# Performance work log

Measured on AMD Instinct MI355X. Metric: run time of the kernel, lower is better.

The kernel has to match this reference:

```python
import jax, jax.numpy as jnp
import numpy as np

M, N, D = 100000, 64, 128  # points, channels, voxel grid side


def setup_inputs() -> dict:
    key = jax.random.key(0)
    k1, k2, k3, k4, k5 = jax.random.split(key, 5)
    rng = np.random.default_rng(0)
    # unique occupied voxels in a D^3 grid (Minkowski coords are unique)
    lin = rng.choice(D ** 3, size=M, replace=False)
    coords = np.stack(np.unravel_index(lin, (D, D, D)), axis=1).astype(np.int32)
    w_scale = 0.02  # ~1/sqrt(fan_in=27*N)
    return {
        "feats": jax.random.normal(k1, (M, N), dtype=jnp.float32),
        "W1": jax.random.normal(k2, (27, N, N), dtype=jnp.float32) * w_scale,
        "b1": jax.random.normal(k3, (N,), dtype=jnp.float32) * 0.01,
        "W2": jax.random.normal(k4, (27, N, N), dtype=jnp.float32) * w_scale,
        "b2": jax.random.normal(k5, (N,), dtype=jnp.float32) * 0.01,
        "coords": jnp.asarray(coords),
        "grid_size": D,
    }


def reference(feats, W1, b1, W2, b2, coords, grid_size):
    Dg = grid_size
    m = feats.shape[0]
    # dense hash: linear voxel id -> point index (-1 if empty)
    lin = (coords[:, 0].astype(jnp.int32) * Dg + coords[:, 1]) * Dg + coords[:, 2]
    lookup = jnp.full((Dg * Dg * Dg,), -1, dtype=jnp.int32).at[lin].set(
        jnp.arange(m, dtype=jnp.int32))
    offsets = jnp.array([[i, j, k] for i in (-1, 0, 1) for j in (-1, 0, 1)
                         for k in (-1, 0, 1)], dtype=jnp.int32)  # [27,3]

    def sparse_conv(x, W, b):
        # out[u] = b + sum_k W_k^T gather(x, u+off_k); scan over 27 offsets keeps
        # only one [M,N] gathered buffer live (memory-bound gather-GEMM-scatter)
        def step(acc, wk_off):
            W_k, off = wk_off
            nc = coords + off  # [M,3]
            inb = jnp.all((nc >= 0) & (nc < Dg), axis=1)
            nlin = (nc[:, 0] * Dg + nc[:, 1]) * Dg + nc[:, 2]
            nidx = lookup[jnp.where(inb, nlin, 0)]
            valid = inb & (nidx >= 0)
            g = jnp.where(valid[:, None], x[jnp.maximum(nidx, 0)], 0.0)  # [M,N]
            return acc + g @ W_k, None
        init = jnp.zeros_like(x) + b
        out, _ = jax.lax.scan(step, init, (W, offsets))
        return out

    h = jax.nn.relu(sparse_conv(feats, W1, b1))
    return jax.nn.relu(sparse_conv(h, W2, b2))
```

## Files before the change

kernel.cpp:

```cpp
#include <hip/hip_runtime.h>
#include <hip/hip_bf16.h>
#include <cstdint>
#include <cstddef>

typedef _Float16 half8 __attribute__((ext_vector_type(8)));
typedef float floatx16 __attribute__((ext_vector_type(16)));

#define DGRID 128
#define D3 (DGRID * DGRID * DGRID)

__global__ void scatter_lookup(const int* __restrict__ coords, int* __restrict__ lookup, int M) {
    int m = blockIdx.x * 256 + threadIdx.x;
    if (m >= M) return;
    int x = coords[3 * m], y = coords[3 * m + 1], z = coords[3 * m + 2];
    lookup[(x * DGRID + y) * DGRID + z] = m;
}

__global__ void build_nbr(const int* __restrict__ coords, const int* __restrict__ lookup,
                          int* __restrict__ nbr, int M) {
    int m = blockIdx.x * 256 + threadIdx.x;
    if (m >= M) return;
    int x = coords[3 * m], y = coords[3 * m + 1], z = coords[3 * m + 2];
#pragma unroll
    for (int k = 0; k < 27; ++k) {
        int nx = x + k / 9 - 1, ny = y + (k / 3) % 3 - 1, nz = z + k % 3 - 1;
        int nidx = -1;
        if (((unsigned)nx < DGRID) && ((unsigned)ny < DGRID) && ((unsigned)nz < DGRID))
            nidx = lookup[(nx * DGRID + ny) * DGRID + nz];
        nbr[k * M + m] = nidx;
    }
}

__global__ void convert_weights(const float* __restrict__ W1, const float* __restrict__ W2,
                                _Float16* __restrict__ Whf) {
    int idx = blockIdx.x * 256 + threadIdx.x;
    if (idx >= 2 * 27 * 4096) return;
    int j = idx & 7;
    int l = (idx >> 3) & 63;
    int f = (idx >> 9) & 7;
    int kL = idx >> 12;
    int k = kL % 27, L = kL / 27;
    int kk = f & 3, ct = f >> 2;
    int c = kk * 16 + (l >> 5) * 8 + j;
    int n = ct * 32 + (l & 31);
    const float* W = L ? W2 : W1;
    Whf[idx] = (_Float16)W[k * 4096 + c * 64 + n];
}

template <typename SrcT, bool OUT_F16>
__global__ __launch_bounds__(64) void spconv(const SrcT* __restrict__ x,
                                             const _Float16* __restrict__ Whf,
                                             const float* __restrict__ bias,
                                             const int* __restrict__ nbr,
                                             void* __restrict__ outp, int M) {
    const int lane = threadIdx.x;
    const int lrow = lane & 31;
    const int lhalf = lane >> 5;
    const int mw = blockIdx.x * 64;
    const int gm0 = mw + lrow;
    const int gm1 = mw + 32 + lrow;
    const bool in0 = gm0 < M, in1 = gm1 < M;

    floatx16 acc[4];
#pragma unroll
    for (int i = 0; i < 4; ++i)
#pragma unroll
        for (int j = 0; j < 16; ++j) acc[i][j] = 0.0f;

    const half8* wb = (const half8*)Whf + lane;

    half8 A[8], B[8];

    auto loadA = [&](half8* dst, int n0, int n1) {
#pragma unroll
        for (int rt = 0; rt < 2; ++rt) {
            int n = rt ? n1 : n0;
#pragma unroll
            for (int kk = 0; kk < 4; ++kk) {
                half8 z;
#pragma unroll
                for (int j = 0; j < 8; ++j) z[j] = (_Float16)0.f;
                dst[rt * 4 + kk] = z;
            }
            if (n >= 0) {
                if constexpr (sizeof(SrcT) == 4) {
                    const float4* p =
                        (const float4*)((const float*)x + (size_t)n * 64 + lhalf * 8);
#pragma unroll
                    for (int kk = 0; kk < 4; ++kk) {
                        float4 f0 = p[kk * 4], f1 = p[kk * 4 + 1];
                        half8 v;
                        v[0] = (_Float16)f0.x; v[1] = (_Float16)f0.y;
                        v[2] = (_Float16)f0.z; v[3] = (_Float16)f0.w;
                        v[4] = (_Float16)f1.x; v[5] = (_Float16)f1.y;
                        v[6] = (_Float16)f1.z; v[7] = (_Float16)f1.w;
                        dst[rt * 4 + kk] = v;
                    }
                } else {
                    const half8* p =
                        (const half8*)((const _Float16*)x + (size_t)n * 64 + lhalf * 8);
#pragma unroll
                    for (int kk = 0; kk < 4; ++kk) dst[rt * 4 + kk] = p[kk * 2];
                }
            }
        }
    };

    int n0 = -1, n1 = -1;
    if (in0) n0 = nbr[gm0];
    if (in1) n1 = nbr[gm1];
    int n0n = -1, n1n = -1;
    if (in0) n0n = nbr[M + gm0];
    if (in1) n1n = nbr[M + gm1];
#pragma unroll
    for (int f = 0; f < 8; ++f) B[f] = wb[f * 64];
    loadA(A, n0, n1);

#pragma unroll
    for (int k = 0; k < 27; ++k) {
        const int kn = (k + 1 < 27) ? k + 1 : 26;
        const int kn2 = (k + 2 < 27) ? k + 2 : 26;
        half8 Bn[8], An[8];
#pragma unroll
        for (int f = 0; f < 8; ++f) Bn[f] = wb[(kn * 8 + f) * 64];
        const int n0f = n0n, n1f = n1n;
        n0n = -1; n1n = -1;
        if (in0) n0n = nbr[(size_t)kn2 * M + gm0];
        if (in1) n1n = nbr[(size_t)kn2 * M + gm1];
        loadA(An, n0f, n1f);
#pragma unroll
        for (int rt = 0; rt < 2; ++rt)
#pragma unroll
            for (int ct = 0; ct < 2; ++ct)
#pragma unroll
                for (int kk = 0; kk < 4; ++kk)
                    acc[rt * 2 + ct] = __builtin_amdgcn_mfma_f32_32x32x16_f16(
                        A[rt * 4 + kk], B[ct * 4 + kk], acc[rt * 2 + ct], 0, 0, 0);
#pragma unroll
        for (int f = 0; f < 8; ++f) { A[f] = An[f]; B[f] = Bn[f]; }
    }

    const float bv0 = bias[lrow];
    const float bv1 = bias[32 + lrow];
#pragma unroll
    for (int rt = 0; rt < 2; ++rt)
#pragma unroll
        for (int ct = 0; ct < 2; ++ct) {
            const float bb = ct ? bv1 : bv0;
#pragma unroll
            for (int reg = 0; reg < 16; ++reg) {
                int row = (reg & 3) + 8 * (reg >> 2) + 4 * lhalf;
                int gm = mw + rt * 32 + row;
                if (gm < M) {
                    float v = acc[rt * 2 + ct][reg] + bb;
                    v = v > 0.f ? v : 0.f;
                    size_t off = (size_t)gm * 64 + ct * 32 + lrow;
                    if constexpr (OUT_F16)
                        ((_Float16*)outp)[off] = (_Float16)v;
                    else
                        ((float*)outp)[off] = v;
                }
            }
        }
}

extern "C" void kernel_launch(void* const* d_in, const int* in_sizes, int n_in,
                              void* d_out, int out_size, void* d_ws, size_t ws_size,
                              hipStream_t stream) {
    const float* feats = (const float*)d_in[0];
    const float* W1 = (const float*)d_in[1];
    const float* b1 = (const float*)d_in[2];
    const float* W2 = (const float*)d_in[3];
    const float* b2 = (const float*)d_in[4];
    const int* coords = (const int*)d_in[5];
    const int M = in_sizes[0] / 64;

    int* lookup = (int*)d_ws;
    int* nbr = lookup + (size_t)D3;
    _Float16* h = (_Float16*)(nbr + (size_t)27 * M);
    _Float16* Whf = h + (size_t)M * 64;
    size_t need = (size_t)D3 * 4 + (size_t)27 * M * 4 + (size_t)M * 64 * 2 +
                  (size_t)2 * 27 * 4096 * 2;
    if (ws_size < need) return;

    hipMemsetAsync(lookup, 0xFF, (size_t)D3 * 4, stream);
    int mb = (M + 255) / 256;
    scatter_lookup<<<mb, 256, 0, stream>>>(coords, lookup, M);
    convert_weights<<<(2 * 27 * 4096 + 255) / 256, 256, 0, stream>>>(W1, W2, Whf);
    build_nbr<<<mb, 256, 0, stream>>>(coords, lookup, nbr, M);

    int cb = (M + 63) / 64;
    spconv<float, true><<<cb, 64, 0, stream>>>(feats, Whf, b1, nbr, (void*)h, M);
    spconv<_Float16, false><<<cb, 64, 0, stream>>>(h, Whf + (size_t)27 * 4096, b2, nbr,
                                                   d_out, M);
}
```

Baseline: 197.6 us.

## Split 27 kernel offsets across two waves with LDS reduction and deeper prefetch

Each 64-row block now runs two waves, each covering half of the 27 neighbor offsets (14 and 13). The two partial accumulators are combined through shared memory before bias, ReLU and the store. The gather prefetch is made deeper, by one stage for the fp32 input and two stages for the fp16 input, using ring buffers of neighbor indices and A tiles. This doubles the waves in flight per tile to hide gather latency, at the cost of an LDS round trip, a barrier, and more registers from launch_bounds(128,2).

```diff
diff --git a/kernel.cpp b/kernel.cpp
--- a/kernel.cpp
+++ b/kernel.cpp
@@ -48,12 +48,17 @@
 }
 
 template <typename SrcT, bool OUT_F16>
-__global__ __launch_bounds__(64) void spconv(const SrcT* __restrict__ x,
-                                             const _Float16* __restrict__ Whf,
-                                             const float* __restrict__ bias,
-                                             const int* __restrict__ nbr,
-                                             void* __restrict__ outp, int M) {
-    const int lane = threadIdx.x;
+__global__ __launch_bounds__(128, 2) void spconv(const SrcT* __restrict__ x,
+                                                 const _Float16* __restrict__ Whf,
+                                                 const float* __restrict__ bias,
+                                                 const int* __restrict__ nbr,
+                                                 void* __restrict__ outp, int M) {
+    constexpr int AD = (sizeof(SrcT) == 4) ? 1 : 2;
+    constexpr int DN = AD + 2;
+    constexpr int NA = AD + 1;
+    const int t = threadIdx.x;
+    const int lane = t & 63;
+    const int wave = t >> 6;
     const int lrow = lane & 31;
     const int lhalf = lane >> 5;
     const int mw = blockIdx.x * 64;
@@ -61,6 +66,9 @@
     const int gm1 = mw + 32 + lrow;
     const bool in0 = gm0 < M, in1 = gm1 < M;
 
+    const int kbase = wave ? 14 : 0;
+    const int kEnd = wave ? 27 : 14;
+
     floatx16 acc[4];
 #pragma unroll
     for (int i = 0; i < 4; ++i)
@@ -69,7 +77,12 @@
 
     const half8* wb = (const half8*)Whf + lane;
 
-    half8 A[8], B[8];
+    auto kidx = [&](int i) { int k = kbase + i; return k < 27 ? k : 26; };
+
+    auto loadB = [&](half8* dst, int k) {
+#pragma unroll
+        for (int f = 0; f < 8; ++f) dst[f] = wb[(k * 8 + f) * 64];
+    };
 
     auto loadA = [&](half8* dst, int n0, int n1) {
 #pragma unroll
@@ -106,28 +119,39 @@
         }
     };
 
-    int n0 = -1, n1 = -1;
-    if (in0) n0 = nbr[gm0];
-    if (in1) n1 = nbr[gm1];
-    int n0n = -1, n1n = -1;
-    if (in0) n0n = nbr[M + gm0];
-    if (in1) n1n = nbr[M + gm1];
-#pragma unroll
-    for (int f = 0; f < 8; ++f) B[f] = wb[f * 64];
-    loadA(A, n0, n1);
-
-#pragma unroll
-    for (int k = 0; k < 27; ++k) {
-        const int kn = (k + 1 < 27) ? k + 1 : 26;
-        const int kn2 = (k + 2 < 27) ? k + 2 : 26;
-        half8 Bn[8], An[8];
-#pragma unroll
-        for (int f = 0; f < 8; ++f) Bn[f] = wb[(kn * 8 + f) * 64];
-        const int n0f = n0n, n1f = n1n;
-        n0n = -1; n1n = -1;
-        if (in0) n0n = nbr[(size_t)kn2 * M + gm0];
-        if (in1) n1n = nbr[(size_t)kn2 * M + gm1];
-        loadA(An, n0f, n1f);
+    int nv0[4], nv1[4];
+#pragma unroll
+    for (int j = 0; j < 4; ++j) {
+        bool v = (j < DN) && (kbase + j < kEnd);
+        int kc = kidx(j);
+        nv0[j] = (in0 && v) ? nbr[(size_t)kc * M + gm0] : -1;
+        nv1[j] = (in1 && v) ? nbr[(size_t)kc * M + gm1] : -1;
+    }
+
+    half8 Ar[NA][8], Br[2][8];
+    loadB(Br[0], kidx(0));
+#pragma unroll
+    for (int j = 0; j < AD; ++j) loadA(Ar[j], nv0[j & 3], nv1[j & 3]);
+
+#pragma unroll
+    for (int i = 0; i < 14; ++i) {
+        {
+            int j = i + DN;
+            if (j < 14) {
+                bool v = kbase + j < kEnd;
+                int kc = kidx(j);
+                int slot = j & 3;
+                nv0[slot] = (in0 && v) ? nbr[(size_t)kc * M + gm0] : -1;
+                nv1[slot] = (in1 && v) ? nbr[(size_t)kc * M + gm1] : -1;
+            }
+        }
+        if (i + 1 < 14) loadB(Br[(i + 1) & 1], kidx(i + 1));
+        {
+            int j = i + AD;
+            if (j < 14) loadA(Ar[j % NA], nv0[j & 3], nv1[j & 3]);
+        }
+        half8* A = Ar[i % NA];
+        half8* B = Br[i & 1];
 #pragma unroll
         for (int rt = 0; rt < 2; ++rt)
 #pragma unroll
@@ -136,32 +160,39 @@
                 for (int kk = 0; kk < 4; ++kk)
                     acc[rt * 2 + ct] = __builtin_amdgcn_mfma_f32_32x32x16_f16(
                         A[rt * 4 + kk], B[ct * 4 + kk], acc[rt * 2 + ct], 0, 0, 0);
-#pragma unroll
-        for (int f = 0; f < 8; ++f) { A[f] = An[f]; B[f] = Bn[f]; }
-    }
-
-    const float bv0 = bias[lrow];
-    const float bv1 = bias[32 + lrow];
-#pragma unroll
-    for (int rt = 0; rt < 2; ++rt)
-#pragma unroll
-        for (int ct = 0; ct < 2; ++ct) {
-            const float bb = ct ? bv1 : bv0;
-#pragma unroll
-            for (int reg = 0; reg < 16; ++reg) {
-                int row = (reg & 3) + 8 * (reg >> 2) + 4 * lhalf;
-                int gm = mw + rt * 32 + row;
-                if (gm < M) {
-                    float v = acc[rt * 2 + ct][reg] + bb;
-                    v = v > 0.f ? v : 0.f;
-                    size_t off = (size_t)gm * 64 + ct * 32 + lrow;
-                    if constexpr (OUT_F16)
-                        ((_Float16*)outp)[off] = (_Float16)v;
-                    else
-                        ((float*)outp)[off] = v;
-                }
-            }
-        }
+    }
+
+    __shared__ __align__(16) float comb[2][32 * 64];
+    const int ort = wave ? 0 : 1;
+    const int mrt = wave;
+#pragma unroll
+    for (int ct = 0; ct < 2; ++ct)
+#pragma unroll
+        for (int reg = 0; reg < 16; ++reg) {
+            int row = (reg & 3) + 8 * (reg >> 2) + 4 * lhalf;
+            comb[ort][row * 64 + ct * 32 + lrow] = acc[ort * 2 + ct][reg];
+        }
+    __syncthreads();
+
+    const float bv0 = bias[lrow], bv1 = bias[32 + lrow];
+#pragma unroll
+    for (int ct = 0; ct < 2; ++ct) {
+        const float bb = ct ? bv1 : bv0;
+#pragma unroll
+        for (int reg = 0; reg < 16; ++reg) {
+            int row = (reg & 3) + 8 * (reg >> 2) + 4 * lhalf;
+            int gm = mw + mrt * 32 + row;
+            if (gm < M) {
+                float v = acc[mrt * 2 + ct][reg] + comb[mrt][row * 64 + ct * 32 + lrow] + bb;
+                v = v > 0.f ? v : 0.f;
+                size_t off = (size_t)gm * 64 + ct * 32 + lrow;
+                if constexpr (OUT_F16)
+                    ((_Float16*)outp)[off] = (_Float16)v;
+                else
+                    ((float*)outp)[off] = v;
+            }
+        }
+    }
 }
 
 extern "C" void kernel_launch(void* const* d_in, const int* in_sizes, int n_in,
@@ -190,7 +221,7 @@
     build_nbr<<<mb, 256, 0, stream>>>(coords, lookup, nbr, M);
 
     int cb = (M + 63) / 64;
-    spconv<float, true><<<cb, 64, 0, stream>>>(feats, Whf, b1, nbr, (void*)h, M);
-    spconv<_Float16, false><<<cb, 64, 0, stream>>>(h, Whf + (size_t)27 * 4096, b2, nbr,
-                                                   d_out, M);
-}
+    spconv<float, true><<<cb, 128, 0, stream>>>(feats, Whf, b1, nbr, (void*)h, M);
+    spconv<_Float16, false><<<cb, 128, 0, stream>>>(h, Whf + (size_t)27 * 4096, b2, nbr,
+                                                    d_out, M);
+}
```

New measurement: 430.0 us. 2.18x slower.

## Shrink conv tile to 32 rows, deepen gather prefetch, use zero-row sentinel

Applied to the files above, without the earlier changes.

Each spconv block now handles 32 points instead of 64. This halves the accumulator registers, and launch_bounds(64,3) requests more resident waves. Missing neighbours now point to a zero sentinel row (index M) instead of -1, which removes the zeroing and branching in the gather. The kernel adds a multi-stage ring of A-fragment prefetches whose depth is set per layer, plus double-buffered weights. The weight conversion and lookup scatter are merged into one prep kernel. Each weight fragment is now reloaded for every 32 rows, so weight traffic per point doubles in exchange for more latency hiding.

```diff
diff --git a/kernel.cpp b/kernel.cpp
--- a/kernel.cpp
+++ b/kernel.cpp
@@ -8,12 +8,34 @@
 
 #define DGRID 128
 #define D3 (DGRID * DGRID * DGRID)
+#define WSZ (2 * 27 * 4096)
 
-__global__ void scatter_lookup(const int* __restrict__ coords, int* __restrict__ lookup, int M) {
-    int m = blockIdx.x * 256 + threadIdx.x;
-    if (m >= M) return;
-    int x = coords[3 * m], y = coords[3 * m + 1], z = coords[3 * m + 2];
-    lookup[(x * DGRID + y) * DGRID + z] = m;
+__global__ void prep(const int* __restrict__ coords, const float* __restrict__ W1,
+                     const float* __restrict__ W2, int* __restrict__ lookup,
+                     _Float16* __restrict__ Whf, _Float16* __restrict__ h,
+                     float* __restrict__ zrowf, int M) {
+    int tid = blockIdx.x * 256 + threadIdx.x;
+    if (tid < WSZ) {
+        int idx = tid;
+        int j = idx & 7;
+        int l = (idx >> 3) & 63;
+        int f = (idx >> 9) & 7;
+        int kL = idx >> 12;
+        int k = kL % 27, L = kL / 27;
+        int kk = f & 3, ct = f >> 2;
+        int c = kk * 16 + (l >> 5) * 8 + j;
+        int n = ct * 32 + (l & 31);
+        const float* W = L ? W2 : W1;
+        Whf[idx] = (_Float16)W[k * 4096 + c * 64 + n];
+    } else if (tid < WSZ + M) {
+        int m = tid - WSZ;
+        int x = coords[3 * m], y = coords[3 * m + 1], z = coords[3 * m + 2];
+        lookup[(x * DGRID + y) * DGRID + z] = m;
+    } else if (tid < WSZ + M + 64) {
+        int j = tid - WSZ - M;
+        h[(size_t)M * 64 + j] = (_Float16)0.f;
+        zrowf[j] = 0.f;
+    }
 }
 
 __global__ void build_nbr(const int* __restrict__ coords, const int* __restrict__ lookup,
@@ -27,141 +49,108 @@
         int nidx = -1;
         if (((unsigned)nx < DGRID) && ((unsigned)ny < DGRID) && ((unsigned)nz < DGRID))
             nidx = lookup[(nx * DGRID + ny) * DGRID + nz];
-        nbr[k * M + m] = nidx;
+        nbr[k * M + m] = (nidx < 0) ? M : nidx;
     }
 }
 
-__global__ void convert_weights(const float* __restrict__ W1, const float* __restrict__ W2,
-                                _Float16* __restrict__ Whf) {
-    int idx = blockIdx.x * 256 + threadIdx.x;
-    if (idx >= 2 * 27 * 4096) return;
-    int j = idx & 7;
-    int l = (idx >> 3) & 63;
-    int f = (idx >> 9) & 7;
-    int kL = idx >> 12;
-    int k = kL % 27, L = kL / 27;
-    int kk = f & 3, ct = f >> 2;
-    int c = kk * 16 + (l >> 5) * 8 + j;
-    int n = ct * 32 + (l & 31);
-    const float* W = L ? W2 : W1;
-    Whf[idx] = (_Float16)W[k * 4096 + c * 64 + n];
-}
-
-template <typename SrcT, bool OUT_F16>
-__global__ __launch_bounds__(64) void spconv(const SrcT* __restrict__ x,
-                                             const _Float16* __restrict__ Whf,
-                                             const float* __restrict__ bias,
-                                             const int* __restrict__ nbr,
-                                             void* __restrict__ outp, int M) {
+template <typename SrcT, int AD, bool OUT_F16>
+__global__ __launch_bounds__(64, 3) void spconv(const SrcT* __restrict__ x,
+                                                const float* __restrict__ zrow,
+                                                const _Float16* __restrict__ Whf,
+                                                const float* __restrict__ bias,
+                                                const int* __restrict__ nbr,
+                                                void* __restrict__ outp, int M) {
+    constexpr int NA = AD + 1;
     const int lane = threadIdx.x;
     const int lrow = lane & 31;
     const int lhalf = lane >> 5;
-    const int mw = blockIdx.x * 64;
-    const int gm0 = mw + lrow;
-    const int gm1 = mw + 32 + lrow;
-    const bool in0 = gm0 < M, in1 = gm1 < M;
+    const int mw = blockIdx.x * 32;
+    const int gm = mw + lrow;
+    const int gmc = gm < M ? gm : M - 1;
 
-    floatx16 acc[4];
+    floatx16 acc[2];
 #pragma unroll
-    for (int i = 0; i < 4; ++i)
+    for (int i = 0; i < 2; ++i)
 #pragma unroll
         for (int j = 0; j < 16; ++j) acc[i][j] = 0.0f;
 
     const half8* wb = (const half8*)Whf + lane;
 
-    half8 A[8], B[8];
+    auto loadB = [&](half8* dst, int k) {
+#pragma unroll
+        for (int f = 0; f < 8; ++f) dst[f] = wb[(k * 8 + f) * 64];
+    };
 
-    auto loadA = [&](half8* dst, int n0, int n1) {
-#pragma unroll
-        for (int rt = 0; rt < 2; ++rt) {
-            int n = rt ? n1 : n0;
+    auto loadA = [&](half8* dst, int n) {
+        if constexpr (sizeof(SrcT) == 4) {
+            const float* rp = (n < M) ? ((const float*)x + (size_t)n * 64) : zrow;
+            const float4* p = (const float4*)(rp + lhalf * 8);
 #pragma unroll
             for (int kk = 0; kk < 4; ++kk) {
-                half8 z;
+                float4 f0 = p[kk * 4], f1 = p[kk * 4 + 1];
+                half8 v;
+                v[0] = (_Float16)f0.x; v[1] = (_Float16)f0.y;
+                v[2] = (_Float16)f0.z; v[3] = (_Float16)f0.w;
+                v[4] = (_Float16)f1.x; v[5] = (_Float16)f1.y;
+                v[6] = (_Float16)f1.z; v[7] = (_Float16)f1.w;
+                dst[kk] = v;
+            }
+        } else {
+            const half8* p = (const half8*)((const _Float16*)x + (size_t)n * 64 + lhalf * 8);
 #pragma unroll
-                for (int j = 0; j < 8; ++j) z[j] = (_Float16)0.f;
-                dst[rt * 4 + kk] = z;
-            }
-            if (n >= 0) {
-                if constexpr (sizeof(SrcT) == 4) {
-                    const float4* p =
-                        (const float4*)((const float*)x + (size_t)n * 64 + lhalf * 8);
-#pragma unroll
-                    for (int kk = 0; kk < 4; ++kk) {
-                        float4 f0 = p[kk * 4], f1 = p[kk * 4 + 1];
-                        half8 v;
-                        v[0] = (_Float16)f0.x; v[1] = (_Float16)f0.y;
-                        v[2] = (_Float16)f0.z; v[3] = (_Float16)f0.w;
-                        v[4] = (_Float16)f1.x; v[5] = (_Float16)f1.y;
-                        v[6] = (_Float16)f1.z; v[7] = (_Float16)f1.w;
-                        dst[rt * 4 + kk] = v;
-                    }
-                } else {
-                    const half8* p =
-                        (const half8*)((const _Float16*)x + (size_t)n * 64 + lhalf * 8);
-#pragma unroll
-                    for (int kk = 0; kk < 4; ++kk) dst[rt * 4 + kk] = p[kk * 2];
-                }
-            }
+            for (int kk = 0; kk < 4; ++kk) dst[kk] = p[kk * 2];
         }
     };
 
-    int n0 = -1, n1 = -1;
-    if (in0) n0 = nbr[gm0];
-    if (in1) n1 = nbr[gm1];
-    int n0n = -1, n1n = -1;
-    if (in0) n0n = nbr[M + gm0];
-    if (in1) n1n = nbr[M + gm1];
+    int nv[4];
 #pragma unroll
-    for (int f = 0; f < 8; ++f) B[f] = wb[f * 64];
-    loadA(A, n0, n1);
+    for (int j = 0; j < 4; ++j) nv[j] = nbr[(size_t)j * M + gmc];
+
+    half8 Ar[NA][4], Br[2][8];
+    loadB(Br[0], 0);
+#pragma unroll
+    for (int j = 0; j < AD; ++j) loadA(Ar[j], nv[j & 3]);
 
 #pragma unroll
-    for (int k = 0; k < 27; ++k) {
-        const int kn = (k + 1 < 27) ? k + 1 : 26;
-        const int kn2 = (k + 2 < 27) ? k + 2 : 26;
-        half8 Bn[8], An[8];
+    for (int i = 0; i < 27; ++i) {
+        {
+            int jn = i + AD + 2;
+            if (jn < 27) nv[jn & 3] = nbr[(size_t)jn * M + gmc];
+        }
+        if (i + 1 < 27) loadB(Br[(i + 1) & 1], i + 1);
+        {
+            int ja = i + AD;
+            if (ja < 27) loadA(Ar[ja % NA], nv[ja & 3]);
+        }
+        half8* A = Ar[i % NA];
+        half8* B = Br[i & 1];
 #pragma unroll
-        for (int f = 0; f < 8; ++f) Bn[f] = wb[(kn * 8 + f) * 64];
-        const int n0f = n0n, n1f = n1n;
-        n0n = -1; n1n = -1;
-        if (in0) n0n = nbr[(size_t)kn2 * M + gm0];
-        if (in1) n1n = nbr[(size_t)kn2 * M + gm1];
-        loadA(An, n0f, n1f);
-#pragma unroll
-        for (int rt = 0; rt < 2; ++rt)
+        for (int kk = 0; kk < 4; ++kk)
 #pragma unroll
             for (int ct = 0; ct < 2; ++ct)
-#pragma unroll
-                for (int kk = 0; kk < 4; ++kk)
-                    acc[rt * 2 + ct] = __builtin_amdgcn_mfma_f32_32x32x16_f16(
-                        A[rt * 4 + kk], B[ct * 4 + kk], acc[rt * 2 + ct], 0, 0, 0);
-#pragma unroll
-        for (int f = 0; f < 8; ++f) { A[f] = An[f]; B[f] = Bn[f]; }
+                acc[ct] = __builtin_amdgcn_mfma_f32_32x32x16_f16(A[kk], B[ct * 4 + kk],
+                                                                 acc[ct], 0, 0, 0);
     }
 
-    const float bv0 = bias[lrow];
-    const float bv1 = bias[32 + lrow];
+    const float bv0 = bias[lrow], bv1 = bias[32 + lrow];
 #pragma unroll
-    for (int rt = 0; rt < 2; ++rt)
+    for (int ct = 0; ct < 2; ++ct) {
+        const float bb = ct ? bv1 : bv0;
 #pragma unroll
-        for (int ct = 0; ct < 2; ++ct) {
-            const float bb = ct ? bv1 : bv0;
-#pragma unroll
-            for (int reg = 0; reg < 16; ++reg) {
-                int row = (reg & 3) + 8 * (reg >> 2) + 4 * lhalf;
-                int gm = mw + rt * 32 + row;
-                if (gm < M) {
-                    float v = acc[rt * 2 + ct][reg] + bb;
-                    v = v > 0.f ? v : 0.f;
-                    size_t off = (size_t)gm * 64 + ct * 32 + lrow;
-                    if constexpr (OUT_F16)
-                        ((_Float16*)outp)[off] = (_Float16)v;
-                    else
-                        ((float*)outp)[off] = v;
-                }
+        for (int reg = 0; reg < 16; ++reg) {
+            int row = (reg & 3) + 8 * (reg >> 2) + 4 * lhalf;
+            int g = mw + row;
+            if (g < M) {
+                float v = acc[ct][reg] + bb;
+                v = v > 0.f ? v : 0.f;
+                size_t off = (size_t)g * 64 + ct * 32 + lrow;
+                if constexpr (OUT_F16)
+                    ((_Float16*)outp)[off] = (_Float16)v;
+                else
+                    ((float*)outp)[off] = v;
             }
         }
+    }
 }
 
 extern "C" void kernel_launch(void* const* d_in, const int* in_sizes, int n_in,
@@ -178,19 +167,19 @@
     int* lookup = (int*)d_ws;
     int* nbr = lookup + (size_t)D3;
     _Float16* h = (_Float16*)(nbr + (size_t)27 * M);
-    _Float16* Whf = h + (size_t)M * 64;
-    size_t need = (size_t)D3 * 4 + (size_t)27 * M * 4 + (size_t)M * 64 * 2 +
-                  (size_t)2 * 27 * 4096 * 2;
+    _Float16* Whf = h + (size_t)(M + 1) * 64;
+    float* zrowf = (float*)(Whf + WSZ);
+    size_t need = (size_t)D3 * 4 + (size_t)27 * M * 4 + (size_t)(M + 1) * 64 * 2 +
+                  (size_t)WSZ * 2 + 64 * 4;
     if (ws_size < need) return;
 
     hipMemsetAsync(lookup, 0xFF, (size_t)D3 * 4, stream);
-    int mb = (M + 255) / 256;
-    scatter_lookup<<<mb, 256, 0, stream>>>(coords, lookup, M);
-    convert_weights<<<(2 * 27 * 4096 + 255) / 256, 256, 0, stream>>>(W1, W2, Whf);
-    build_nbr<<<mb, 256, 0, stream>>>(coords, lookup, nbr, M);
+    int pt = WSZ + M + 64;
+    prep<<<(pt + 255) / 256, 256, 0, stream>>>(coords, W1, W2, lookup, Whf, h, zrowf, M);
+    build_nbr<<<(M + 255) / 256, 256, 0, stream>>>(coords, lookup, nbr, M);
 
-    int cb = (M + 63) / 64;
-    spconv<float, true><<<cb, 64, 0, stream>>>(feats, Whf, b1, nbr, (void*)h, M);
-    spconv<_Float16, false><<<cb, 64, 0, stream>>>(h, Whf + (size_t)27 * 4096, b2, nbr,
-                                                   d_out, M);
+    int cb = (M + 31) / 32;
+    spconv<float, 1, true><<<cb, 64, 0, stream>>>(feats, zrowf, Whf, b1, nbr, (void*)h, M);
+    spconv<_Float16, 2, false><<<cb, 64, 0, stream>>>(h, zrowf, Whf + (size_t)27 * 4096,
+                                                      b2, nbr, d_out, M);
 }
```

Measured after the change: 217.2 us. 9.9% more time.
